# Kernel optimization log

Measured on AMD Instinct MI355X. Metric: run time of the kernel, lower is better.

The kernel has to match this reference:

```python
import jax, jax.numpy as jnp
import numpy as np

N_NODES = 20000
N_EDGES = 320000
IN_DIM = 256
OUT_DIM = 256
H1, H2 = 640, 320


def _linear_params(key, fan_in, fan_out):
    k1, k2 = jax.random.split(key)
    bound = 1.0 / np.sqrt(fan_in)
    w = jax.random.uniform(k1, (fan_in, fan_out), minval=-bound, maxval=bound, dtype=jnp.float32)
    b = jax.random.uniform(k2, (fan_out,), minval=-bound, maxval=bound, dtype=jnp.float32)
    return w, b


def setup_inputs() -> dict:
    key = jax.random.key(0)
    ks = jax.random.split(key, 10)
    features = jax.random.normal(ks[0], (N_NODES, IN_DIM), dtype=jnp.float32)
    edge_index = jax.random.randint(ks[1], (2, N_EDGES), 0, N_NODES, dtype=jnp.int64)
    w1a, b1a = _linear_params(ks[2], IN_DIM, H1)
    w1b, b1b = _linear_params(ks[3], H1, H1)
    w2a, b2a = _linear_params(ks[4], H1, H2)
    w2b, b2b = _linear_params(ks[5], H2, H2)
    w3a, b3a = _linear_params(ks[6], H2, OUT_DIM)
    w3b, b3b = _linear_params(ks[7], OUT_DIM, OUT_DIM)
    wr, br = _linear_params(ks[8], IN_DIM, OUT_DIM)
    return dict(features=features, edge_index=edge_index,
                w1a=w1a, b1a=b1a, w1b=w1b, b1b=b1b,
                w2a=w2a, b2a=b2a, w2b=w2b, b2b=b2b,
                w3a=w3a, b3a=b3a, w3b=w3b, b3b=b3b,
                wr=wr, br=br)


def _gin_layer(x, src, dst, wa, ba, wb, bb):
    # DGL GINConv 'sum': h = (1+eps)*x + sum_{src->dst} x[src], eps=0
    agg = jax.ops.segment_sum(x[src], dst, num_segments=N_NODES)
    h = x + agg
    h = jax.nn.elu(h @ wa + ba)
    h = jax.nn.elu(h @ wb + bb)
    return h


def reference(features, edge_index, w1a, b1a, w1b, b1b, w2a, b2a, w2b, b2b,
              w3a, b3a, w3b, b3b, wr, br):
    src, dst = edge_index[0], edge_index[1]
    res = jax.nn.elu(features @ wr + br)
    x = jax.nn.elu(_gin_layer(features, src, dst, w1a, b1a, w1b, b1b))
    # dropout (p=0.2) omitted: eval mode
    x = jax.nn.elu(_gin_layer(x, src, dst, w2a, b2a, w2b, b2b))
    x = _gin_layer(x, src, dst, w3a, b3a, w3b, b3b)
    return (x, res)
```

## Files before the change

### kernel.cpp

```cpp
#include <hip/hip_runtime.h>
#include <cstdint>
#include <cstddef>

#define NN 20000
#define NE 320000

typedef short short8 __attribute__((ext_vector_type(8)));
typedef float f32x4 __attribute__((ext_vector_type(4)));
typedef unsigned short u16;

__device__ __forceinline__ float b2f(u16 u) {
  union { unsigned int i; float f; } z; z.i = ((unsigned int)u) << 16; return z.f;
}
__device__ __forceinline__ u16 f2b(float f) {
  union { float f; unsigned int i; } z; z.f = f;
  unsigned int r = z.i + 0x7fffu + ((z.i >> 16) & 1u);
  return (u16)(r >> 16);
}
__device__ __forceinline__ float eluf(float v) {
  return v > 0.0f ? v : __expf(v) - 1.0f;
}

__global__ __launch_bounds__(256) void k_prep(
    const float* __restrict__ features, u16* __restrict__ xbf_sliced,
    const int* __restrict__ edst, int* __restrict__ counts,
    const float* __restrict__ wr, const float* __restrict__ w1a,
    const float* __restrict__ w1b, const float* __restrict__ w2a,
    const float* __restrict__ w2b, const float* __restrict__ w3a,
    const float* __restrict__ w3b,
    u16* __restrict__ wrt, u16* __restrict__ w1at, u16* __restrict__ w1bt,
    u16* __restrict__ w2at, u16* __restrict__ w2bt, u16* __restrict__ w3at,
    u16* __restrict__ w3bt) {
  int tid = blockIdx.x * 256 + threadIdx.x;
  if (tid < 1280000) {
    int node = tid >> 6;
    int c4 = (tid & 63) * 4;
    float4 v = *reinterpret_cast<const float4*>(features + (size_t)node * 256 + c4);
    ushort4 o;
    o.x = f2b(v.x); o.y = f2b(v.y); o.z = f2b(v.z); o.w = f2b(v.w);
    int slice = c4 >> 6, within = c4 & 63;
    *reinterpret_cast<ushort4*>(xbf_sliced + (size_t)slice * NN * 64 +
                                (size_t)node * 64 + within) = o;
    return;
  }
  if (tid < 1600000) {
    atomicAdd(&counts[edst[tid - 1280000]], 1);
    return;
  }
  int r = tid - 1600000;
  const float* Ws[7] = {wr, w1a, w1b, w2a, w2b, w3a, w3b};
  u16* Wts[7] = {wrt, w1at, w1bt, w2at, w2bt, w3at, w3bt};
  const int Kd[7] = {256, 256, 640, 640, 320, 320, 256};
  const int Nd[7] = {256, 640, 640, 320, 320, 256, 256};
  const int cnt[7] = {65536, 163840, 409600, 204800, 102400, 81920, 65536};
#pragma unroll
  for (int j = 0; j < 7; ++j) {
    if (r < cnt[j]) {
      int n = r / Kd[j], k = r - n * Kd[j];
      Wts[j][r] = f2b(Ws[j][(size_t)k * Nd[j] + n]);
      return;
    }
    r -= cnt[j];
  }
}

__global__ __launch_bounds__(1024) void k_scan(const int* __restrict__ counts,
                                               int* __restrict__ rs,
                                               int* __restrict__ cur) {
  __shared__ int wsum[16];
  __shared__ int carry_s;
  int t = threadIdx.x;
  int l = t & 63, w = t >> 6;
  if (t == 0) carry_s = 0;
  __syncthreads();
  for (int base = 0; base < NN; base += 4096) {
    int idx = base + t * 4;
    int4 v = {0, 0, 0, 0};
    if (idx < NN) v = *reinterpret_cast<const int4*>(counts + idx);
    int p0 = v.x, p1 = p0 + v.y, p2 = p1 + v.z, p3 = p2 + v.w;
    int incl = p3;
#pragma unroll
    for (int off = 1; off < 64; off <<= 1) {
      int u = __shfl_up(incl, off, 64);
      if (l >= off) incl += u;
    }
    if (l == 63) wsum[w] = incl;
    __syncthreads();
    int carry = carry_s;
    int wpre = 0;
    for (int k2 = 0; k2 < w; ++k2) wpre += wsum[k2];
    int tot = 0;
    if (t == 0)
      for (int k2 = 0; k2 < 16; ++k2) tot += wsum[k2];
    int ex = carry + wpre + incl - p3;
    if (idx < NN) {
      int4 o;
      o.x = ex; o.y = ex + p0; o.z = ex + p1; o.w = ex + p2;
      *reinterpret_cast<int4*>(rs + idx) = o;
      *reinterpret_cast<int4*>(cur + idx) = o;
    }
    __syncthreads();
    if (t == 0) carry_s = carry + tot;
    __syncthreads();
  }
  if (t == 0) rs[NN] = carry_s;
}

__global__ __launch_bounds__(256) void k_scatter(const int* __restrict__ src,
                                                 const int* __restrict__ dst,
                                                 int* __restrict__ cursor,
                                                 int* __restrict__ csr_src, int ne) {
  int i = blockIdx.x * 256 + threadIdx.x;
  if (i >= ne) return;
  int d = dst[i];
  int p = atomicAdd(&cursor[d], 1);
  csr_src[p] = src[i];
}

template <int D, int ACT>
__global__ __launch_bounds__(256) void k_agg(const u16* __restrict__ xs,
                                             const int* __restrict__ rs,
                                             const int* __restrict__ cs,
                                             const float* __restrict__ bias,
                                             u16* __restrict__ h) {
  constexpr int SW = D / 4;
  constexpr int NCs = SW / 8;
  constexpr int NPB = 256 / NCs;
  int b = blockIdx.x;
  int cls = b & 7;
  int slice = cls & 3;
  int half = cls >> 2;
  int t = threadIdx.x;
  int nl = t / NCs, ch = t - nl * NCs;
  if (nl >= NPB) return;
  int node = half * 10000 + (b >> 3) * NPB + nl;
  if (node >= (half ? NN : 10000)) return;
  const u16* xp = xs + (size_t)slice * NN * SW + (size_t)ch * 8;
  float acc[8];
  {
    short8 v = *reinterpret_cast<const short8*>(xp + (size_t)node * SW);
#pragma unroll
    for (int q = 0; q < 8; ++q) acc[q] = b2f((u16)v[q]);
  }
  int e0 = rs[node], e1 = rs[node + 1];
  int e = e0;
  for (; e + 16 <= e1; e += 16) {
    int s[16];
#pragma unroll
    for (int u = 0; u < 16; ++u) s[u] = cs[e + u];
    short8 v[16];
#pragma unroll
    for (int u = 0; u < 16; ++u)
      v[u] = *reinterpret_cast<const short8*>(xp + (size_t)s[u] * SW);
#pragma unroll
    for (int q = 0; q < 8; ++q) {
      float a0 = (b2f((u16)v[0][q]) + b2f((u16)v[1][q])) +
                 (b2f((u16)v[2][q]) + b2f((u16)v[3][q]));
      float a1 = (b2f((u16)v[4][q]) + b2f((u16)v[5][q])) +
                 (b2f((u16)v[6][q]) + b2f((u16)v[7][q]));
      float a2 = (b2f((u16)v[8][q]) + b2f((u16)v[9][q])) +
                 (b2f((u16)v[10][q]) + b2f((u16)v[11][q]));
      float a3 = (b2f((u16)v[12][q]) + b2f((u16)v[13][q])) +
                 (b2f((u16)v[14][q]) + b2f((u16)v[15][q]));
      acc[q] += (a0 + a1) + (a2 + a3);
    }
  }
  for (; e + 8 <= e1; e += 8) {
    int s[8];
#pragma unroll
    for (int u = 0; u < 8; ++u) s[u] = cs[e + u];
    short8 v[8];
#pragma unroll
    for (int u = 0; u < 8; ++u)
      v[u] = *reinterpret_cast<const short8*>(xp + (size_t)s[u] * SW);
#pragma unroll
    for (int q = 0; q < 8; ++q) {
      float a0 = b2f((u16)v[0][q]) + b2f((u16)v[1][q]);
      float a1 = b2f((u16)v[2][q]) + b2f((u16)v[3][q]);
      float a2 = b2f((u16)v[4][q]) + b2f((u16)v[5][q]);
      float a3 = b2f((u16)v[6][q]) + b2f((u16)v[7][q]);
      acc[q] += (a0 + a1) + (a2 + a3);
    }
  }
  for (; e + 4 <= e1; e += 4) {
    int s0 = cs[e], s1 = cs[e + 1], s2 = cs[e + 2], s3 = cs[e + 3];
    short8 v0 = *reinterpret_cast<const short8*>(xp + (size_t)s0 * SW);
    short8 v1 = *reinterpret_cast<const short8*>(xp + (size_t)s1 * SW);
    short8 v2 = *reinterpret_cast<const short8*>(xp + (size_t)s2 * SW);
    short8 v3 = *reinterpret_cast<const short8*>(xp + (size_t)s3 * SW);
#pragma unroll
    for (int q = 0; q < 8; ++q)
      acc[q] += (b2f((u16)v0[q]) + b2f((u16)v1[q])) + (b2f((u16)v2[q]) + b2f((u16)v3[q]));
  }
  for (; e < e1; ++e) {
    int s = cs[e];
    short8 v = *reinterpret_cast<const short8*>(xp + (size_t)s * SW);
#pragma unroll
    for (int q = 0; q < 8; ++q) acc[q] += b2f((u16)v[q]);
  }
  int col0 = slice * SW + ch * 8;
  if (ACT == 1) {
    float4 b0 = *reinterpret_cast<const float4*>(bias + col0);
    float4 b1 = *reinterpret_cast<const float4*>(bias + col0 + 4);
    acc[0] = eluf(acc[0] + b0.x); acc[1] = eluf(acc[1] + b0.y);
    acc[2] = eluf(acc[2] + b0.z); acc[3] = eluf(acc[3] + b0.w);
    acc[4] = eluf(acc[4] + b1.x); acc[5] = eluf(acc[5] + b1.y);
    acc[6] = eluf(acc[6] + b1.z); acc[7] = eluf(acc[7] + b1.w);
  }
  short8 o;
#pragma unroll
  for (int q = 0; q < 8; ++q) o[q] = (short)f2b(acc[q]);
  *reinterpret_cast<short8*>(h + (size_t)node * D + col0) = o;
}

template <int BM, int K, int N, int ACT, bool OUTF32, bool INS, int OSW>
__global__ __launch_bounds__(256) void k_gemm(const u16* __restrict__ A,
                                              const u16* __restrict__ Bt,
                                              const float* __restrict__ bias,
                                              void* __restrict__ outp, int M) {
  constexpr int NBY = (N + 127) / 128;
  constexpr int NK = K / 32;
  constexpr int ABUF = BM * 32;
  constexpr int BUFSZ = ABUF + 4096;
  constexpr int MI = BM / 32;
  constexpr int LPT = BM / 64 + 2;
  __shared__ __align__(16) u16 smem[3 * BUFSZ];
  int t = threadIdx.x;
  int l = t & 63, w = t >> 6;
  int lm = l & 15, lk = l >> 4;

  int nb = gridDim.x;
  int q8 = nb >> 3, r8 = nb & 7;
  int orig = blockIdx.x;
  int xcd = orig & 7, idx = orig >> 3;
  int wg = (xcd < r8 ? xcd * (q8 + 1) : r8 * (q8 + 1) + (xcd - r8) * q8) + idx;
  int m0 = (wg / NBY) * BM;
  int n0 = (wg % NBY) * 128;
  int wm = (w >> 1) * (BM / 2), wn = (w & 1) * 64;

  f32x4 acc[MI][4];
#pragma unroll
  for (int i = 0; i < MI; ++i)
#pragma unroll
    for (int j = 0; j < 4; ++j)
#pragma unroll
      for (int qq = 0; qq < 4; ++qq) acc[i][j][qq] = 0.0f;

  auto stage = [&](int buf, int kt) {
    int k0 = kt * 32;
    u16* As = smem + buf * BUFSZ;
    u16* Bs = As + ABUF;
#pragma unroll
    for (int it = 0; it < BM / 64; ++it) {
      int c = it * 256 + t;
      int row = c >> 2;
      int kc = (c & 3) ^ ((c >> 3) & 3);
      int ra = m0 + row; ra = ra < M ? ra : M - 1;
      const u16* ga;
      if (INS)
        ga = A + (size_t)(k0 >> 6) * NN * 64 + (size_t)ra * 64 + (k0 & 63) + kc * 8;
      else
        ga = A + (size_t)ra * K + k0 + kc * 8;
      __builtin_amdgcn_global_load_lds(
          (const __attribute__((address_space(1))) void*)ga,
          (__attribute__((address_space(3))) void*)(As + c * 8), 16, 0, 0);
    }
#pragma unroll
    for (int it = 0; it < 2; ++it) {
      int c = it * 256 + t;
      int row = c >> 2;
      int kc = (c & 3) ^ ((c >> 3) & 3);
      int rb = n0 + row; rb = rb < N ? rb : N - 1;
      const u16* gb = Bt + (size_t)rb * K + k0 + kc * 8;
      __builtin_amdgcn_global_load_lds(
          (const __attribute__((address_space(1))) void*)gb,
          (__attribute__((address_space(3))) void*)(Bs + c * 8), 16, 0, 0);
    }
  };

  int kidx = (lk ^ ((lm >> 1) & 3)) * 8;

  stage(0, 0);
  asm volatile("" ::: "memory");
  stage(1, 1);
  asm volatile("" ::: "memory");
  stage(2, 2);
  int buf = 0;
  for (int kt = 0; kt < NK; ++kt) {
    int rem = NK - 1 - kt;
    if (rem >= 2)
      asm volatile("s_waitcnt vmcnt(%0)" ::"n"(2 * LPT) : "memory");
    else if (rem == 1)
      asm volatile("s_waitcnt vmcnt(%0)" ::"n"(LPT) : "memory");
    else
      asm volatile("s_waitcnt vmcnt(0)" ::: "memory");
    __builtin_amdgcn_s_barrier();
    asm volatile("" ::: "memory");
    const u16* As = smem + buf * BUFSZ;
    const u16* Bs = As + ABUF;
    short8 af[MI], bf[4];
#pragma unroll
    for (int i = 0; i < MI; ++i)
      af[i] = *reinterpret_cast<const short8*>(As + (wm + i * 16 + lm) * 32 + kidx);
#pragma unroll
    for (int j = 0; j < 4; ++j)
      bf[j] = *reinterpret_cast<const short8*>(Bs + (wn + j * 16 + lm) * 32 + kidx);
    __builtin_amdgcn_s_setprio(1);
#pragma unroll
    for (int i = 0; i < MI; ++i)
#pragma unroll
      for (int j = 0; j < 4; ++j)
        acc[i][j] = __builtin_amdgcn_mfma_f32_16x16x32_bf16(af[i], bf[j], acc[i][j], 0, 0, 0);
    __builtin_amdgcn_s_setprio(0);
    asm volatile("s_waitcnt lgkmcnt(0)" ::: "memory");
    __builtin_amdgcn_s_barrier();
    asm volatile("" ::: "memory");
    if (kt + 3 < NK) stage(buf, kt + 3);
    buf = (buf == 2) ? 0 : buf + 1;
  }

  if (!OUTF32) {
    u16* ep = smem + w * (BM / 2) * 64;
#pragma unroll
    for (int j = 0; j < 4; ++j) {
      int col = n0 + wn + j * 16 + lm;
      float bv = (ACT > 0) ? bias[col < N ? col : N - 1] : 0.0f;
#pragma unroll
      for (int i = 0; i < MI; ++i)
#pragma unroll
        for (int qq = 0; qq < 4; ++qq) {
          float v = acc[i][j][qq];
          if (ACT > 0) { v += bv; v = eluf(v); }
          if (ACT == 2) v = eluf(v);
          ep[(i * 16 + lk * 4 + qq) * 64 + j * 16 + lm] = f2b(v);
        }
    }
    __syncthreads();
    u16* op = (u16*)outp;
#pragma unroll
    for (int u = 0; u < BM / 16; ++u) {
      int rrow = m0 + wm + u * 8 + (l >> 3);
      int col = n0 + wn + (l & 7) * 8;
      if (rrow < M && col < N) {
        short8 val = *reinterpret_cast<const short8*>(ep + u * 512 + l * 8);
        if (OSW) {
          int slice = col / OSW, within = col - slice * OSW;
          *reinterpret_cast<short8*>(op + (size_t)slice * NN * OSW +
                                     (size_t)rrow * OSW + within) = val;
        } else {
          *reinterpret_cast<short8*>(op + (size_t)rrow * N + col) = val;
        }
      }
    }
  } else {
    float* op = (float*)outp;
#pragma unroll
    for (int j = 0; j < 4; ++j) {
      int col = n0 + wn + j * 16 + lm;
      if (col >= N) continue;
      float bv = (ACT > 0) ? bias[col] : 0.0f;
#pragma unroll
      for (int i = 0; i < MI; ++i) {
        int rb = m0 + wm + i * 16 + lk * 4;
#pragma unroll
        for (int qq = 0; qq < 4; ++qq) {
          int rr = rb + qq;
          if (rr >= M) continue;
          float v = acc[i][j][qq];
          if (ACT > 0) { v += bv; v = eluf(v); }
          if (ACT == 2) v = eluf(v);
          op[(size_t)rr * N + col] = v;
        }
      }
    }
  }
}

extern "C" void kernel_launch(void* const* d_in, const int* in_sizes, int n_in,
                              void* d_out, int out_size, void* d_ws, size_t ws_size,
                              hipStream_t stream) {
  const float* features = (const float*)d_in[0];
  const int* eidx = (const int*)d_in[1];
  const float* w1a = (const float*)d_in[2];
  const float* b1a = (const float*)d_in[3];
  const float* w1b = (const float*)d_in[4];
  const float* b1b = (const float*)d_in[5];
  const float* w2a = (const float*)d_in[6];
  const float* b2a = (const float*)d_in[7];
  const float* w2b = (const float*)d_in[8];
  const float* b2b = (const float*)d_in[9];
  const float* w3a = (const float*)d_in[10];
  const float* b3a = (const float*)d_in[11];
  const float* w3b = (const float*)d_in[12];
  const float* b3b = (const float*)d_in[13];
  const float* wr = (const float*)d_in[14];
  const float* br = (const float*)d_in[15];

  char* ws = (char*)d_ws;
  u16* bufA = (u16*)(ws);
  u16* bufB = (u16*)(ws + 25600000);
  u16* wrt = (u16*)(ws + 51200000);
  u16* w1at = wrt + 256 * 256;
  u16* w1bt = w1at + 640 * 256;
  u16* w2at = w1bt + 640 * 640;
  u16* w2bt = w2at + 320 * 640;
  u16* w3at = w2bt + 320 * 320;
  u16* w3bt = w3at + 256 * 320;
  int* row_start = (int*)(ws + 53387264);
  int* cursor = row_start + 20004;
  int* csr_src = cursor + NN;
  int* counts = csr_src + NE;

  const int* esrc = eidx;
  const int* edst = eidx + NE;

  hipMemsetAsync(counts, 0, NN * sizeof(int), stream);
  k_prep<<<10523, 256, 0, stream>>>(features, bufA, edst, counts, wr, w1a, w1b,
                                    w2a, w2b, w3a, w3b, wrt, w1at, w1bt, w2at,
                                    w2bt, w3at, w3bt);
  k_scan<<<1, 1024, 0, stream>>>(counts, row_start, cursor);
  k_scatter<<<(NE + 255) / 256, 256, 0, stream>>>(esrc, edst, cursor, csr_src, NE);

  float* out_x = (float*)d_out;
  float* out_res = (float*)d_out + (size_t)NN * 256;

  k_gemm<64, 256, 256, 1, true, true, 0><<<dim3(313 * 2), 256, 0, stream>>>(bufA, wrt, br, out_res, NN);
  k_agg<256, 0><<<8 * 313, 256, 0, stream>>>(bufA, row_start, csr_src, nullptr, bufB);
  k_gemm<128, 256, 640, 1, false, false, 0><<<dim3(157 * 5), 256, 0, stream>>>(bufB, w1at, b1a, bufA, NN);
  k_gemm<128, 640, 640, 2, false, false, 0><<<dim3(157 * 5), 256, 0, stream>>>(bufA, w1bt, b1b, bufB, NN);
  k_gemm<128, 640, 320, 0, false, false, 80><<<dim3(157 * 3), 256, 0, stream>>>(bufB, w2at, nullptr, bufA, NN);
  k_agg<320, 1><<<8 * 400, 256, 0, stream>>>(bufA, row_start, csr_src, b2a, bufB);
  k_gemm<64, 320, 320, 2, false, false, 0><<<dim3(313 * 3), 256, 0, stream>>>(bufB, w2bt, b2b, bufA, NN);
  k_gemm<64, 320, 256, 0, false, false, 64><<<dim3(313 * 2), 256, 0, stream>>>(bufA, w3at, nullptr, bufB, NN);
  k_agg<256, 1><<<8 * 313, 256, 0, stream>>>(bufB, row_start, csr_src, b3a, bufA);
  k_gemm<64, 256, 256, 1, true, false, 0><<<dim3(313 * 2), 256, 0, stream>>>(bufA, w3bt, b3b, out_x, NN);
}
```

Baseline: 255.7 us.

## Merge residual and final GEMMs into one launch; tune pipeline slots

Adds a dual-problem GEMM kernel that computes the residual projection and the final layer-3 projection in a single launch, splitting workgroups between the two problems. The residual GEMM moves from the start to the end, so the sliced input features are kept in a dedicated buffer. The buffer offsets are reorganized to hold it. The pipeline depth becomes a template parameter, and the two 128-row layer-1 GEMMs drop from three to two LDS stages, likely to raise occupancy. This saves one kernel launch and fills the GPU better on the small final GEMM, at the cost of less latency hiding in the two-stage GEMMs.

```diff
diff --git a/kernel.cpp b/kernel.cpp
--- a/kernel.cpp
+++ b/kernel.cpp
@@ -213,7 +213,7 @@
   *reinterpret_cast<short8*>(h + (size_t)node * D + col0) = o;
 }
 
-template <int BM, int K, int N, int ACT, bool OUTF32, bool INS, int OSW>
+template <int BM, int K, int N, int ACT, bool OUTF32, bool INS, int OSW, int SLOTS>
 __global__ __launch_bounds__(256) void k_gemm(const u16* __restrict__ A,
                                               const u16* __restrict__ Bt,
                                               const float* __restrict__ bias,
@@ -224,7 +224,7 @@
   constexpr int BUFSZ = ABUF + 4096;
   constexpr int MI = BM / 32;
   constexpr int LPT = BM / 64 + 2;
-  __shared__ __align__(16) u16 smem[3 * BUFSZ];
+  __shared__ __align__(16) u16 smem[SLOTS * BUFSZ];
   int t = threadIdx.x;
   int l = t & 63, w = t >> 6;
   int lm = l & 15, lk = l >> 4;
@@ -280,11 +280,185 @@
 
   int kidx = (lk ^ ((lm >> 1) & 3)) * 8;
 
-  stage(0, 0);
-  asm volatile("" ::: "memory");
-  stage(1, 1);
-  asm volatile("" ::: "memory");
-  stage(2, 2);
+#pragma unroll
+  for (int s = 0; s < SLOTS; ++s) {
+    stage(s, s);
+    asm volatile("" ::: "memory");
+  }
+  int buf = 0;
+  for (int kt = 0; kt < NK; ++kt) {
+    int rem = NK - 1 - kt;
+    if (SLOTS == 3) {
+      if (rem >= 2)
+        asm volatile("s_waitcnt vmcnt(%0)" ::"n"(2 * LPT) : "memory");
+      else if (rem == 1)
+        asm volatile("s_waitcnt vmcnt(%0)" ::"n"(LPT) : "memory");
+      else
+        asm volatile("s_waitcnt vmcnt(0)" ::: "memory");
+    } else {
+      if (rem >= 1)
+        asm volatile("s_waitcnt vmcnt(%0)" ::"n"(LPT) : "memory");
+      else
+        asm volatile("s_waitcnt vmcnt(0)" ::: "memory");
+    }
+    __builtin_amdgcn_s_barrier();
+    asm volatile("" ::: "memory");
+    const u16* As = smem + buf * BUFSZ;
+    const u16* Bs = As + ABUF;
+    short8 af[MI], bf[4];
+#pragma unroll
+    for (int i = 0; i < MI; ++i)
+      af[i] = *reinterpret_cast<const short8*>(As + (wm + i * 16 + lm) * 32 + kidx);
+#pragma unroll
+    for (int j = 0; j < 4; ++j)
+      bf[j] = *reinterpret_cast<const short8*>(Bs + (wn + j * 16 + lm) * 32 + kidx);
+    __builtin_amdgcn_s_setprio(1);
+#pragma unroll
+    for (int i = 0; i < MI; ++i)
+#pragma unroll
+      for (int j = 0; j < 4; ++j)
+        acc[i][j] = __builtin_amdgcn_mfma_f32_16x16x32_bf16(af[i], bf[j], acc[i][j], 0, 0, 0);
+    __builtin_amdgcn_s_setprio(0);
+    asm volatile("s_waitcnt lgkmcnt(0)" ::: "memory");
+    __builtin_amdgcn_s_barrier();
+    asm volatile("" ::: "memory");
+    if (kt + SLOTS < NK) stage(buf, kt + SLOTS);
+    buf = (buf == SLOTS - 1) ? 0 : buf + 1;
+  }
+
+  if (!OUTF32) {
+    u16* ep = smem + w * (BM / 2) * 64;
+#pragma unroll
+    for (int j = 0; j < 4; ++j) {
+      int col = n0 + wn + j * 16 + lm;
+      float bv = (ACT > 0) ? bias[col < N ? col : N - 1] : 0.0f;
+#pragma unroll
+      for (int i = 0; i < MI; ++i)
+#pragma unroll
+        for (int qq = 0; qq < 4; ++qq) {
+          float v = acc[i][j][qq];
+          if (ACT > 0) { v += bv; v = eluf(v); }
+          if (ACT == 2) v = eluf(v);
+          ep[(i * 16 + lk * 4 + qq) * 64 + j * 16 + lm] = f2b(v);
+        }
+    }
+    __syncthreads();
+    u16* op = (u16*)outp;
+#pragma unroll
+    for (int u = 0; u < BM / 16; ++u) {
+      int rrow = m0 + wm + u * 8 + (l >> 3);
+      int col = n0 + wn + (l & 7) * 8;
+      if (rrow < M && col < N) {
+        short8 val = *reinterpret_cast<const short8*>(ep + u * 512 + l * 8);
+        if (OSW) {
+          int slice = col / OSW, within = col - slice * OSW;
+          *reinterpret_cast<short8*>(op + (size_t)slice * NN * OSW +
+                                     (size_t)rrow * OSW + within) = val;
+        } else {
+          *reinterpret_cast<short8*>(op + (size_t)rrow * N + col) = val;
+        }
+      }
+    }
+  } else {
+    float* op = (float*)outp;
+#pragma unroll
+    for (int j = 0; j < 4; ++j) {
+      int col = n0 + wn + j * 16 + lm;
+      if (col >= N) continue;
+      float bv = (ACT > 0) ? bias[col] : 0.0f;
+#pragma unroll
+      for (int i = 0; i < MI; ++i) {
+        int rb = m0 + wm + i * 16 + lk * 4;
+#pragma unroll
+        for (int qq = 0; qq < 4; ++qq) {
+          int rr = rb + qq;
+          if (rr >= M) continue;
+          float v = acc[i][j][qq];
+          if (ACT > 0) { v += bv; v = eluf(v); }
+          if (ACT == 2) v = eluf(v);
+          op[(size_t)rr * N + col] = v;
+        }
+      }
+    }
+  }
+}
+
+__global__ __launch_bounds__(256) void k_gemmd(
+    const u16* __restrict__ A0, const u16* __restrict__ Bt0,
+    const float* __restrict__ bias0, float* __restrict__ out0,
+    const u16* __restrict__ A1, const u16* __restrict__ Bt1,
+    const float* __restrict__ bias1, float* __restrict__ out1) {
+  constexpr int K = 256, N = 256, BM = 64;
+  constexpr int NBY = 2, NK = 8, NT0 = 626;
+  constexpr int ABUF = BM * 32, BUFSZ = ABUF + 4096, MI = 2, LPT = 3;
+  constexpr int SLOTS = 3;
+  __shared__ __align__(16) u16 smem[SLOTS * BUFSZ];
+  int t = threadIdx.x;
+  int l = t & 63, w = t >> 6;
+  int lm = l & 15, lk = l >> 4;
+
+  int nb = gridDim.x;
+  int q8 = nb >> 3, r8 = nb & 7;
+  int orig = blockIdx.x;
+  int xcd = orig & 7, idx = orig >> 3;
+  int wg = (xcd < r8 ? xcd * (q8 + 1) : r8 * (q8 + 1) + (xcd - r8) * q8) + idx;
+  bool second = wg >= NT0;
+  int tt = second ? wg - NT0 : wg;
+  const u16* A = second ? A1 : A0;
+  const u16* Bt = second ? Bt1 : Bt0;
+  const float* bias = second ? bias1 : bias0;
+  float* op = second ? out1 : out0;
+
+  int m0 = (tt / NBY) * BM;
+  int n0 = (tt % NBY) * 128;
+  int wm = (w >> 1) * (BM / 2), wn = (w & 1) * 64;
+
+  f32x4 acc[MI][4];
+#pragma unroll
+  for (int i = 0; i < MI; ++i)
+#pragma unroll
+    for (int j = 0; j < 4; ++j)
+#pragma unroll
+      for (int qq = 0; qq < 4; ++qq) acc[i][j][qq] = 0.0f;
+
+  auto stage = [&](int buf, int kt) {
+    int k0 = kt * 32;
+    u16* As = smem + buf * BUFSZ;
+    u16* Bs = As + ABUF;
+    {
+      int c = t;
+      int row = c >> 2;
+      int kc = (c & 3) ^ ((c >> 3) & 3);
+      int ra = m0 + row; ra = ra < NN ? ra : NN - 1;
+      const u16* ga;
+      if (second)
+        ga = A + (size_t)(k0 >> 6) * NN * 64 + (size_t)ra * 64 + (k0 & 63) + kc * 8;
+      else
+        ga = A + (size_t)ra * K + k0 + kc * 8;
+      __builtin_amdgcn_global_load_lds(
+          (const __attribute__((address_space(1))) void*)ga,
+          (__attribute__((address_space(3))) void*)(As + c * 8), 16, 0, 0);
+    }
+#pragma unroll
+    for (int it = 0; it < 2; ++it) {
+      int c = it * 256 + t;
+      int row = c >> 2;
+      int kc = (c & 3) ^ ((c >> 3) & 3);
+      int rb = n0 + row; rb = rb < N ? rb : N - 1;
+      const u16* gb = Bt + (size_t)rb * K + k0 + kc * 8;
+      __builtin_amdgcn_global_load_lds(
+          (const __attribute__((address_space(1))) void*)gb,
+          (__attribute__((address_space(3))) void*)(Bs + c * 8), 16, 0, 0);
+    }
+  };
+
+  int kidx = (lk ^ ((lm >> 1) & 3)) * 8;
+
+#pragma unroll
+  for (int s = 0; s < SLOTS; ++s) {
+    stage(s, s);
+    asm volatile("" ::: "memory");
+  }
   int buf = 0;
   for (int kt = 0; kt < NK; ++kt) {
     int rem = NK - 1 - kt;
@@ -315,62 +489,23 @@
     asm volatile("s_waitcnt lgkmcnt(0)" ::: "memory");
     __builtin_amdgcn_s_barrier();
     asm volatile("" ::: "memory");
-    if (kt + 3 < NK) stage(buf, kt + 3);
-    buf = (buf == 2) ? 0 : buf + 1;
-  }
-
-  if (!OUTF32) {
-    u16* ep = smem + w * (BM / 2) * 64;
-#pragma unroll
-    for (int j = 0; j < 4; ++j) {
-      int col = n0 + wn + j * 16 + lm;
-      float bv = (ACT > 0) ? bias[col < N ? col : N - 1] : 0.0f;
-#pragma unroll
-      for (int i = 0; i < MI; ++i)
-#pragma unroll
-        for (int qq = 0; qq < 4; ++qq) {
-          float v = acc[i][j][qq];
-          if (ACT > 0) { v += bv; v = eluf(v); }
-          if (ACT == 2) v = eluf(v);
-          ep[(i * 16 + lk * 4 + qq) * 64 + j * 16 + lm] = f2b(v);
-        }
-    }
-    __syncthreads();
-    u16* op = (u16*)outp;
-#pragma unroll
-    for (int u = 0; u < BM / 16; ++u) {
-      int rrow = m0 + wm + u * 8 + (l >> 3);
-      int col = n0 + wn + (l & 7) * 8;
-      if (rrow < M && col < N) {
-        short8 val = *reinterpret_cast<const short8*>(ep + u * 512 + l * 8);
-        if (OSW) {
-          int slice = col / OSW, within = col - slice * OSW;
-          *reinterpret_cast<short8*>(op + (size_t)slice * NN * OSW +
-                                     (size_t)rrow * OSW + within) = val;
-        } else {
-          *reinterpret_cast<short8*>(op + (size_t)rrow * N + col) = val;
-        }
-      }
-    }
-  } else {
-    float* op = (float*)outp;
-#pragma unroll
-    for (int j = 0; j < 4; ++j) {
-      int col = n0 + wn + j * 16 + lm;
-      if (col >= N) continue;
-      float bv = (ACT > 0) ? bias[col] : 0.0f;
-#pragma unroll
-      for (int i = 0; i < MI; ++i) {
-        int rb = m0 + wm + i * 16 + lk * 4;
-#pragma unroll
-        for (int qq = 0; qq < 4; ++qq) {
-          int rr = rb + qq;
-          if (rr >= M) continue;
-          float v = acc[i][j][qq];
-          if (ACT > 0) { v += bv; v = eluf(v); }
-          if (ACT == 2) v = eluf(v);
-          op[(size_t)rr * N + col] = v;
-        }
+    if (kt + SLOTS < NK) stage(buf, kt + SLOTS);
+    buf = (buf == SLOTS - 1) ? 0 : buf + 1;
+  }
+
+#pragma unroll
+  for (int j = 0; j < 4; ++j) {
+    int col = n0 + wn + j * 16 + lm;
+    float bv = bias[col];
+#pragma unroll
+    for (int i = 0; i < MI; ++i) {
+      int rb = m0 + wm + i * 16 + lk * 4;
+#pragma unroll
+      for (int qq = 0; qq < 4; ++qq) {
+        int rr = rb + qq;
+        if (rr >= NN) continue;
+        float v = eluf(acc[i][j][qq] + bv);
+        op[(size_t)rr * N + col] = v;
       }
     }
   }
@@ -397,16 +532,17 @@
   const float* br = (const float*)d_in[15];
 
   char* ws = (char*)d_ws;
-  u16* bufA = (u16*)(ws);
-  u16* bufB = (u16*)(ws + 25600000);
-  u16* wrt = (u16*)(ws + 51200000);
+  u16* bufX = (u16*)(ws);
+  u16* bufA = (u16*)(ws + 10240000);
+  u16* bufB = (u16*)(ws + 35840000);
+  u16* wrt = (u16*)(ws + 61440000);
   u16* w1at = wrt + 256 * 256;
   u16* w1bt = w1at + 640 * 256;
   u16* w2at = w1bt + 640 * 640;
   u16* w2bt = w2at + 320 * 640;
   u16* w3at = w2bt + 320 * 320;
   u16* w3bt = w3at + 256 * 320;
-  int* row_start = (int*)(ws + 53387264);
+  int* row_start = (int*)(ws + 63700992);
   int* cursor = row_start + 20004;
   int* csr_src = cursor + NN;
   int* counts = csr_src + NE;
@@ -415,7 +551,7 @@
   const int* edst = eidx + NE;
 
   hipMemsetAsync(counts, 0, NN * sizeof(int), stream);
-  k_prep<<<10523, 256, 0, stream>>>(features, bufA, edst, counts, wr, w1a, w1b,
+  k_prep<<<10523, 256, 0, stream>>>(features, bufX, edst, counts, wr, w1a, w1b,
                                     w2a, w2b, w3a, w3b, wrt, w1at, w1bt, w2at,
                                     w2bt, w3at, w3bt);
   k_scan<<<1, 1024, 0, stream>>>(counts, row_start, cursor);
@@ -424,14 +560,14 @@
   float* out_x = (float*)d_out;
   float* out_res = (float*)d_out + (size_t)NN * 256;
 
-  k_gemm<64, 256, 256, 1, true, true, 0><<<dim3(313 * 2), 256, 0, stream>>>(bufA, wrt, br, out_res, NN);
-  k_agg<256, 0><<<8 * 313, 256, 0, stream>>>(bufA, row_start, csr_src, nullptr, bufB);
-  k_gemm<128, 256, 640, 1, false, false, 0><<<dim3(157 * 5), 256, 0, stream>>>(bufB, w1at, b1a, bufA, NN);
-  k_gemm<128, 640, 640, 2, false, false, 0><<<dim3(157 * 5), 256, 0, stream>>>(bufA, w1bt, b1b, bufB, NN);
-  k_gemm<128, 640, 320, 0, false, false, 80><<<dim3(157 * 3), 256, 0, stream>>>(bufB, w2at, nullptr, bufA, NN);
-  k_agg<320, 1><<<8 * 400, 256, 0, stream>>>(bufA, row_start, csr_src, b2a, bufB);
-  k_gemm<64, 320, 320, 2, false, false, 0><<<dim3(313 * 3), 256, 0, stream>>>(bufB, w2bt, b2b, bufA, NN);
-  k_gemm<64, 320, 256, 0, false, false, 64><<<dim3(313 * 2), 256, 0, stream>>>(bufA, w3at, nullptr, bufB, NN);
-  k_agg<256, 1><<<8 * 313, 256, 0, stream>>>(bufB, row_start, csr_src, b3a, bufA);
-  k_gemm<64, 256, 256, 1, true, false, 0><<<dim3(313 * 2), 256, 0, stream>>>(bufA, w3bt, b3b, out_x, NN);
-}
+  k_agg<256, 0><<<8 * 313, 256, 0, stream>>>(bufX, row_start, csr_src, nullptr, bufA);
+  k_gemm<128, 256, 640, 1, false, false, 0, 2><<<dim3(157 * 5), 256, 0, stream>>>(bufA, w1at, b1a, bufB, NN);
+  k_gemm<128, 640, 640, 2, false, false, 0, 2><<<dim3(157 * 5), 256, 0, stream>>>(bufB, w1bt, b1b, bufA, NN);
+  k_gemm<128, 640, 320, 0, false, false, 80, 3><<<dim3(157 * 3), 256, 0, stream>>>(bufA, w2at, nullptr, bufB, NN);
+  k_agg<320, 1><<<8 * 400, 256, 0, stream>>>(bufB, row_start, csr_src, b2a, bufA);
+  k_gemm<64, 320, 320, 2, false, false, 0, 3><<<dim3(313 * 3), 256, 0, stream>>>(bufA, w2bt, b2b, bufB, NN);
+  k_gemm<64, 320, 256, 0, false, false, 64, 3><<<dim3(313 * 2), 256, 0, stream>>>(bufB, w3at, nullptr, bufA, NN);
+  k_agg<256, 1><<<8 * 313, 256, 0, stream>>>(bufA, row_start, csr_src, b3a, bufB);
+  k_gemmd<<<dim3(626 * 2), 256, 0, stream>>>(bufB, w3bt, b3b, out_x,
+                                             bufX, wrt, br, out_res);
+}
```

Result: faster. 245.4 us (-4.1%).
